# Kernel tuning notes

Measured on AMD Instinct MI355X. Metric: run time of the kernel, lower is better.

## Reference

```python
import jax, jax.numpy as jnp
import numpy as np

B, T, C, NH = 4, 2048, 1024, 16
D = C // NH  # 64


def setup_inputs() -> dict:
    key = jax.random.key(0)
    ks = jax.random.split(key, 6)
    x = jax.random.normal(ks[0], (B, T, C), dtype=jnp.float32)
    # realistic RoPE tables: interleaved cos/sin over T positions, D head dim
    inv_freq = 1.0 / (10000.0 ** (np.arange(0, D, 2, dtype=np.float32) / D))
    ang = np.arange(T, dtype=np.float32)[:, None] * inv_freq[None, :]  # (T, D/2)
    ang = np.repeat(ang, 2, axis=-1)  # (T, D) interleaved
    pe_cos = jnp.asarray(np.cos(ang))[None, None]  # (1,1,T,D)
    pe_sin = jnp.asarray(np.sin(ang))[None, None]
    pe_scale = jax.random.uniform(ks[1], (1, 1, T, D), dtype=jnp.float32, minval=0.5, maxval=1.5)
    mask = 0.1 * jax.random.normal(ks[2], (1, B, T, T), dtype=jnp.float32)
    w_qkv = jax.random.normal(ks[3], (3 * C, C), dtype=jnp.float32) * (C ** -0.5)
    b_qkv = jax.random.normal(ks[4], (3 * C,), dtype=jnp.float32) * 0.02
    return {"x": x, "pe_cos": pe_cos, "pe_sin": pe_sin, "pe_scale": pe_scale,
            "mask": mask, "w_qkv": w_qkv, "b_qkv": b_qkv}


def _rotate_interleaved(u):
    # even positions <- -odd, odd positions <- even (RoPE interleave)
    u2 = u.reshape(u.shape[:-1] + (-1, 2))
    rot = jnp.stack([-u2[..., 1], u2[..., 0]], axis=-1)
    return rot.reshape(u.shape)


def reference(x, pe_cos, pe_sin, pe_scale, mask, w_qkv, b_qkv):
    b, t, c = x.shape
    qkv = x @ w_qkv.T + b_qkv  # (b, t, 3c)
    q, k, v = jnp.split(qkv, 3, axis=-1)
    # (b, t, nh, d) -> (b, nh, t, d)
    to_heads = lambda u: u.reshape(b, t, NH, D).transpose(0, 2, 1, 3)
    q, k, v = to_heads(q), to_heads(k), to_heads(v)
    # pe tensors (1,1,t,d) broadcast over (b,nh,t,d)
    q = (q * pe_cos + _rotate_interleaved(q) * pe_sin) * pe_scale
    k = (k * pe_cos + _rotate_interleaved(k) * pe_sin) / pe_scale
    scale = 1.0 / ((2.0 * D) ** 0.5)  # original uses scale=1/sqrt(2d)
    scores = jnp.einsum('bhqd,bhkd->bhqk', q, k) * scale
    # torch layout was (nh, b, t, t) + mask (1, b, t, t): mask broadcasts over heads
    scores = scores + jnp.swapaxes(mask, 0, 1)  # mask -> (b, 1, t, t)
    attn = jax.nn.softmax(scores, axis=-1)
    out = jnp.einsum('bhqk,bhkd->bhqd', attn, v)  # (b, nh, t, d)
    return out.transpose(0, 2, 1, 3).reshape(b, t, c)
```

## Files before the change

kernel.cpp:

```cpp
#include <hip/hip_runtime.h>
#include <math.h>

#define NB 4
#define NT 2048
#define NC 1024
#define NHEADS 16
#define HDIM 64

typedef __attribute__((ext_vector_type(8))) _Float16 half8v;
typedef __attribute__((ext_vector_type(4))) float f32x4;

__device__ inline unsigned short f2h(float f) {
    _Float16 h = (_Float16)f;
    return __builtin_bit_cast(unsigned short, h);
}

#define AS1C(p) ((const __attribute__((address_space(1))) unsigned int*)(unsigned long long)(const void*)(p))
#define AS3P(p) ((__attribute__((address_space(3))) unsigned int*)(unsigned int)(unsigned long long)(void*)(p))
#define GLL16(gp, lp) __builtin_amdgcn_global_load_lds(AS1C(gp), AS3P(lp), 16, 0, 0)

__global__ __launch_bounds__(256) void conv_f16_kernel(
    const float* __restrict__ in, unsigned short* __restrict__ out, int n4)
{
    const int i = blockIdx.x * 256 + threadIdx.x;
    if (i >= n4) return;
    const float4 f = ((const float4*)in)[i];
    ushort4 h;
    h.x = f2h(f.x); h.y = f2h(f.y); h.z = f2h(f.z); h.w = f2h(f.w);
    ((ushort4*)out)[i] = h;
}

__global__ __launch_bounds__(256) void qkv_gemm_kernel(
    const unsigned short* __restrict__ xf, const unsigned short* __restrict__ wf,
    const float* __restrict__ bias, const float* __restrict__ pe_cos,
    const float* __restrict__ pe_sin, const float* __restrict__ pe_scale,
    unsigned short* __restrict__ qb, unsigned short* __restrict__ kb,
    unsigned short* __restrict__ vtb)
{
    __shared__ __align__(16) unsigned short Ah[128 * 32];
    __shared__ __align__(16) unsigned short Bh[128 * 32];

    const int tid = threadIdx.x;
    const int w = tid >> 6, lane = tid & 63;
    const int g = lane >> 4, fr = lane & 15;
    const int wr = w >> 1, wc = w & 1;

    const int bid = blockIdx.x;
    const int s = (bid & 7) * 192 + (bid >> 3);
    const int m0 = (s & 63) * 128, n0 = (s >> 6) * 128;

    const int c0 = tid, c1 = tid + 256;
    const int r0 = c0 >> 2, r1 = c1 >> 2;
    const int cb0 = ((c0 & 3) * 16) ^ (((r0 >> 1) & 3) << 4);
    const int cb1 = ((c1 & 3) * 16) ^ (((r1 >> 1) & 3) << 4);
    const unsigned short* px0 = xf + (size_t)(m0 + r0) * NC + (cb0 >> 1);
    const unsigned short* px1 = xf + (size_t)(m0 + r1) * NC + (cb1 >> 1);
    const unsigned short* pw0 = wf + (size_t)(n0 + r0) * NC + (cb0 >> 1);
    const unsigned short* pw1 = wf + (size_t)(n0 + r1) * NC + (cb1 >> 1);

    f32x4 acc[4][4];
#pragma unroll
    for (int m = 0; m < 4; ++m)
#pragma unroll
        for (int n = 0; n < 4; ++n) acc[m][n] = (f32x4){0.f, 0.f, 0.f, 0.f};

    for (int k0 = 0; k0 < NC; k0 += 32) {
        __syncthreads();
        GLL16(px0 + k0, (char*)Ah + c0 * 16);
        GLL16(px1 + k0, (char*)Ah + c1 * 16);
        GLL16(pw0 + k0, (char*)Bh + c0 * 16);
        GLL16(pw1 + k0, (char*)Bh + c1 * 16);
        __syncthreads();

        half8v a_f[4], b_f[4];
#pragma unroll
        for (int m = 0; m < 4; ++m) {
            const int r = wr * 64 + m * 16 + fr;
            const int off = r * 64 + ((g * 16) ^ (((r >> 1) & 3) << 4));
            a_f[m] = *(const half8v*)((const char*)Ah + off);
        }
#pragma unroll
        for (int n = 0; n < 4; ++n) {
            const int r = wc * 64 + n * 16 + fr;
            const int off = r * 64 + ((g * 16) ^ (((r >> 1) & 3) << 4));
            b_f[n] = *(const half8v*)((const char*)Bh + off);
        }
#pragma unroll
        for (int m = 0; m < 4; ++m)
#pragma unroll
            for (int n = 0; n < 4; ++n)
                acc[m][n] = __builtin_amdgcn_mfma_f32_16x16x32_f16(a_f[m], b_f[n], acc[m][n], 0, 0, 0);
    }

#pragma unroll
    for (int n = 0; n < 4; ++n) {
        const int col = n0 + wc * 64 + n * 16 + fr;
        const int part = col >> 10;
        const int hh = (col & 1023) >> 6;
        const int dd = col & 63;
        const float bv = bias[col];
#pragma unroll
        for (int m = 0; m < 4; ++m) {
            const int row0 = m0 + wr * 64 + m * 16 + 4 * g;
            const int bb = row0 >> 11;
            const int t0 = row0 & 2047;
            if (part < 2) {
                unsigned short* outp = (part == 0) ? qb : kb;
#pragma unroll
                for (int j = 0; j < 4; ++j) {
                    const int t = t0 + j;
                    float val = acc[m][n][j] + bv;
                    const float partner = __shfl_xor(val, 1, 64);
                    const int pidx = t * HDIM + dd;
                    const float cc = pe_cos[pidx], ss = pe_sin[pidx], sc = pe_scale[pidx];
                    const float r = (dd & 1) ? (val * cc + partner * ss)
                                             : (val * cc - partner * ss);
                    val = (part == 0) ? (r * sc) : (r / sc);
                    outp[(((size_t)bb * NHEADS + hh) * NT + t) * HDIM + dd] = f2h(val);
                }
            } else {
                ushort4 sv;
                sv.x = f2h(acc[m][n][0] + bv);
                sv.y = f2h(acc[m][n][1] + bv);
                sv.z = f2h(acc[m][n][2] + bv);
                sv.w = f2h(acc[m][n][3] + bv);
                *(ushort4*)&vtb[(((size_t)bb * NHEADS + hh) * HDIM + dd) * NT + t0] = sv;
            }
        }
    }
}

__global__ __launch_bounds__(256) void attn_mfma_kernel(
    const unsigned short* __restrict__ qb, const unsigned short* __restrict__ kb,
    const unsigned short* __restrict__ vtb, const float* __restrict__ mask,
    float* __restrict__ out)
{
    __shared__ __align__(16) unsigned short Qs[64 * 64];
    __shared__ __align__(16) unsigned short Ks[64 * 64];
    __shared__ __align__(16) unsigned short Vs[64 * 64];
    __shared__ __align__(16) unsigned short Ps[4][16 * 64];

    const int tid = threadIdx.x;
    const int w = tid >> 6, lane = tid & 63;
    const int g = lane >> 4, fr = lane & 15;

    const int bid = blockIdx.x;
    const int s = (bid & 7) * 256 + (bid >> 3);
    const int q0 = (s & 31) * 64;
    const int h = (s >> 5) & 15;
    const int b = s >> 9;

    const size_t bh = (size_t)b * NHEADS + h;
    const unsigned short* qp = qb + (bh * NT + q0) * HDIM;
    const unsigned short* kp = kb + bh * NT * HDIM;
    const unsigned short* vtp = vtb + bh * HDIM * NT;
    const float* mp = mask + ((size_t)b * NT + q0) * NT;

    {
        const int c0 = tid, c1 = tid + 256;
        const int r0 = c0 >> 3, cbq0 = ((c0 & 7) * 16) ^ ((r0 & 7) << 4);
        const int r1 = c1 >> 3, cbq1 = ((c1 & 7) * 16) ^ ((r1 & 7) << 4);
        GLL16(qp + r0 * HDIM + (cbq0 >> 1), (char*)Qs + c0 * 16);
        GLL16(qp + r1 * HDIM + (cbq1 >> 1), (char*)Qs + c1 * 16);
    }
    __syncthreads();
    half8v qf[2];
    {
        const int r = w * 16 + fr;
#pragma unroll
        for (int kk = 0; kk < 2; ++kk) {
            const int off = r * 128 + ((g * 16 + kk * 64) ^ ((r & 7) << 4));
            qf[kk] = *(const half8v*)((const char*)Qs + off);
        }
    }

    f32x4 acc[4];
    float li[4], mi[4];
#pragma unroll
    for (int j = 0; j < 4; ++j) {
        li[j] = 0.f; mi[j] = -3.0e38f;
        acc[j] = (f32x4){0.f, 0.f, 0.f, 0.f};
    }
    const float scl = 0.08838834764831845f;

    for (int kt = 0; kt < NT / 64; ++kt) {
        __syncthreads();
        {
            const unsigned short* ktp = kp + kt * 64 * HDIM;
#pragma unroll
            for (int half = 0; half < 2; ++half) {
                const int c = tid + half * 256;
                const int r = c >> 3;
                const int cb = ((c & 7) * 16) ^ ((r & 7) << 4);
                GLL16(ktp + r * HDIM + (cb >> 1), (char*)Ks + c * 16);
                GLL16(vtp + (size_t)r * NT + kt * 64 + (cb >> 1), (char*)Vs + c * 16);
            }
        }
        __syncthreads();

        f32x4 S[4];
#pragma unroll
        for (int nt = 0; nt < 4; ++nt) {
            S[nt] = (f32x4){0.f, 0.f, 0.f, 0.f};
            const int r = nt * 16 + fr;
#pragma unroll
            for (int kk = 0; kk < 2; ++kk) {
                const int off = r * 128 + ((g * 16 + kk * 64) ^ ((r & 7) << 4));
                const half8v kf = *(const half8v*)((const char*)Ks + off);
                S[nt] = __builtin_amdgcn_mfma_f32_16x16x32_f16(qf[kk], kf, S[nt], 0, 0, 0);
            }
        }

        float sv[4][4], rmj[4];
#pragma unroll
        for (int j = 0; j < 4; ++j) {
            const int qrow = w * 16 + 4 * g + j;
            const float* mrow = mp + (size_t)qrow * NT + kt * 64 + fr;
#pragma unroll
            for (int nt = 0; nt < 4; ++nt)
                sv[j][nt] = fmaf(S[nt][j], scl, mrow[nt * 16]);
            rmj[j] = fmaxf(fmaxf(sv[j][0], sv[j][1]), fmaxf(sv[j][2], sv[j][3]));
        }

        float worst = fmaxf(fmaxf(rmj[0] - mi[0], rmj[1] - mi[1]),
                            fmaxf(rmj[2] - mi[2], rmj[3] - mi[3]));
        if (!__all(worst <= 8.f)) {
#pragma unroll
            for (int j = 0; j < 4; ++j) {
                float rm = rmj[j];
                rm = fmaxf(rm, __shfl_xor(rm, 1, 64));
                rm = fmaxf(rm, __shfl_xor(rm, 2, 64));
                rm = fmaxf(rm, __shfl_xor(rm, 4, 64));
                rm = fmaxf(rm, __shfl_xor(rm, 8, 64));
                const float mnew = fmaxf(mi[j], rm);
                const float alpha = __expf(mi[j] - mnew);
                li[j] *= alpha;
                acc[0][j] *= alpha; acc[1][j] *= alpha;
                acc[2][j] *= alpha; acc[3][j] *= alpha;
                mi[j] = mnew;
            }
        }

#pragma unroll
        for (int j = 0; j < 4; ++j) {
            const int prow = 4 * g + j;
            float ps = 0.f;
#pragma unroll
            for (int nt = 0; nt < 4; ++nt) {
                const float p = __expf(sv[j][nt] - mi[j]);
                const int off = prow * 128 + ((nt * 32 + fr * 2) ^ ((prow & 7) << 4));
                *(unsigned short*)((char*)Ps[w] + off) = f2h(p);
                ps += p;
            }
            li[j] += ps;
        }

        half8v pf[2];
#pragma unroll
        for (int kk = 0; kk < 2; ++kk) {
            const int off = fr * 128 + ((g * 16 + kk * 64) ^ ((fr & 7) << 4));
            pf[kk] = *(const half8v*)((const char*)Ps[w] + off);
        }
#pragma unroll
        for (int dt = 0; dt < 4; ++dt) {
            const int d = dt * 16 + fr;
#pragma unroll
            for (int kk = 0; kk < 2; ++kk) {
                const int off = d * 128 + ((g * 16 + kk * 64) ^ ((d & 7) << 4));
                const half8v vf = *(const half8v*)((const char*)Vs + off);
                acc[dt] = __builtin_amdgcn_mfma_f32_16x16x32_f16(pf[kk], vf, acc[dt], 0, 0, 0);
            }
        }
    }

#pragma unroll
    for (int j = 0; j < 4; ++j) {
        float lt = li[j];
        lt += __shfl_xor(lt, 1, 64);
        lt += __shfl_xor(lt, 2, 64);
        lt += __shfl_xor(lt, 4, 64);
        lt += __shfl_xor(lt, 8, 64);
        const float inv = 1.f / lt;
        const int t = q0 + w * 16 + 4 * g + j;
        float* op = out + (((size_t)b * NT + t) * NHEADS + h) * HDIM;
#pragma unroll
        for (int dt = 0; dt < 4; ++dt) op[dt * 16 + fr] = acc[dt][j] * inv;
    }
}

extern "C" void kernel_launch(void* const* d_in, const int* in_sizes, int n_in,
                              void* d_out, int out_size, void* d_ws, size_t ws_size,
                              hipStream_t stream) {
    const float* x        = (const float*)d_in[0];
    const float* pe_cos   = (const float*)d_in[1];
    const float* pe_sin   = (const float*)d_in[2];
    const float* pe_scale = (const float*)d_in[3];
    const float* mask     = (const float*)d_in[4];
    const float* w_qkv    = (const float*)d_in[5];
    const float* b_qkv    = (const float*)d_in[6];
    float* out = (float*)d_out;

    unsigned short* ws = (unsigned short*)d_ws;
    const size_t PER = (size_t)NB * NHEADS * NT * HDIM;
    unsigned short* qbuf = ws;
    unsigned short* kbuf = ws + PER;
    unsigned short* vtbuf = ws + 2 * PER;
    unsigned short* xbuf = ws + 3 * PER;
    unsigned short* wbuf = ws + 4 * PER;

    conv_f16_kernel<<<8192, 256, 0, stream>>>(x, xbuf, (NB * NT * NC) / 4);
    conv_f16_kernel<<<3072, 256, 0, stream>>>(w_qkv, wbuf, (3 * NC * NC) / 4);
    qkv_gemm_kernel<<<1536, 256, 0, stream>>>(xbuf, wbuf, b_qkv,
                                              pe_cos, pe_sin, pe_scale,
                                              qbuf, kbuf, vtbuf);
    attn_mfma_kernel<<<2048, 256, 0, stream>>>(qbuf, kbuf, vtbuf, mask, out);
}
```

Before: 277.2 us.

## Enlarge attention Q tile to 256 rows per block and stream mask as fp16

Each wave now handles 64 query rows (four 16-row sub-tiles) instead of 16, so every K/V tile loaded into LDS is reused across four times as many queries. The grid drops from 2048 to 512 blocks, Q fragments load straight from global memory into registers, and launch bounds request two blocks per CU. The mask is converted to fp16 by an extra pass into the workspace region that held x, halving the attention kernel's mask reads. The trade-offs are a large register footprint from 16 accumulator tiles, fewer blocks for latency hiding, and an extra full read and write of the mask in the conversion kernel.

```diff
diff --git a/kernel.cpp b/kernel.cpp
--- a/kernel.cpp
+++ b/kernel.cpp
@@ -13,6 +13,9 @@
 __device__ inline unsigned short f2h(float f) {
     _Float16 h = (_Float16)f;
     return __builtin_bit_cast(unsigned short, h);
+}
+__device__ inline float h2f(unsigned short u) {
+    return (float)__builtin_bit_cast(_Float16, u);
 }
 
 #define AS1C(p) ((const __attribute__((address_space(1))) unsigned int*)(unsigned long long)(const void*)(p))
@@ -130,57 +133,47 @@
     }
 }
 
-__global__ __launch_bounds__(256) void attn_mfma_kernel(
+__global__ __launch_bounds__(256, 2) void attn_mfma_kernel(
     const unsigned short* __restrict__ qb, const unsigned short* __restrict__ kb,
-    const unsigned short* __restrict__ vtb, const float* __restrict__ mask,
+    const unsigned short* __restrict__ vtb, const unsigned short* __restrict__ m16,
     float* __restrict__ out)
 {
-    __shared__ __align__(16) unsigned short Qs[64 * 64];
     __shared__ __align__(16) unsigned short Ks[64 * 64];
     __shared__ __align__(16) unsigned short Vs[64 * 64];
-    __shared__ __align__(16) unsigned short Ps[4][16 * 64];
+    __shared__ __align__(16) unsigned short Ps[4][64 * 64];
 
     const int tid = threadIdx.x;
     const int w = tid >> 6, lane = tid & 63;
     const int g = lane >> 4, fr = lane & 15;
 
     const int bid = blockIdx.x;
-    const int s = (bid & 7) * 256 + (bid >> 3);
-    const int q0 = (s & 31) * 64;
-    const int h = (s >> 5) & 15;
-    const int b = s >> 9;
+    const int s = (bid & 7) * 64 + (bid >> 3);
+    const int q0 = (s & 7) * 256;
+    const int h = (s >> 3) & 15;
+    const int b = s >> 7;
 
     const size_t bh = (size_t)b * NHEADS + h;
-    const unsigned short* qp = qb + (bh * NT + q0) * HDIM;
+    const unsigned short* qp = qb + (bh * NT + q0 + w * 64) * HDIM;
     const unsigned short* kp = kb + bh * NT * HDIM;
     const unsigned short* vtp = vtb + bh * HDIM * NT;
-    const float* mp = mask + ((size_t)b * NT + q0) * NT;
-
-    {
-        const int c0 = tid, c1 = tid + 256;
-        const int r0 = c0 >> 3, cbq0 = ((c0 & 7) * 16) ^ ((r0 & 7) << 4);
-        const int r1 = c1 >> 3, cbq1 = ((c1 & 7) * 16) ^ ((r1 & 7) << 4);
-        GLL16(qp + r0 * HDIM + (cbq0 >> 1), (char*)Qs + c0 * 16);
-        GLL16(qp + r1 * HDIM + (cbq1 >> 1), (char*)Qs + c1 * 16);
-    }
-    __syncthreads();
-    half8v qf[2];
-    {
-        const int r = w * 16 + fr;
-#pragma unroll
-        for (int kk = 0; kk < 2; ++kk) {
-            const int off = r * 128 + ((g * 16 + kk * 64) ^ ((r & 7) << 4));
-            qf[kk] = *(const half8v*)((const char*)Qs + off);
-        }
-    }
-
-    f32x4 acc[4];
-    float li[4], mi[4];
-#pragma unroll
-    for (int j = 0; j < 4; ++j) {
-        li[j] = 0.f; mi[j] = -3.0e38f;
-        acc[j] = (f32x4){0.f, 0.f, 0.f, 0.f};
-    }
+    const unsigned short* mp = m16 + ((size_t)b * NT + q0 + w * 64) * NT;
+
+    half8v qf[4][2];
+#pragma unroll
+    for (int m = 0; m < 4; ++m)
+#pragma unroll
+        for (int kk = 0; kk < 2; ++kk)
+            qf[m][kk] = *(const half8v*)(qp + (m * 16 + fr) * HDIM + kk * 32 + g * 8);
+
+    f32x4 acc[4][4];
+    float li[4][4], mi[4][4];
+#pragma unroll
+    for (int m = 0; m < 4; ++m)
+#pragma unroll
+        for (int j = 0; j < 4; ++j) {
+            li[m][j] = 0.f; mi[m][j] = -3.0e38f;
+            acc[m][j] = (f32x4){0.f, 0.f, 0.f, 0.f};
+        }
     const float scl = 0.08838834764831845f;
 
     for (int kt = 0; kt < NT / 64; ++kt) {
@@ -198,94 +191,114 @@
         }
         __syncthreads();
 
-        f32x4 S[4];
+        half8v kf[4][2];
 #pragma unroll
         for (int nt = 0; nt < 4; ++nt) {
-            S[nt] = (f32x4){0.f, 0.f, 0.f, 0.f};
             const int r = nt * 16 + fr;
 #pragma unroll
             for (int kk = 0; kk < 2; ++kk) {
-                const int off = r * 128 + ((g * 16 + kk * 64) ^ ((r & 7) << 4));
-                const half8v kf = *(const half8v*)((const char*)Ks + off);
-                S[nt] = __builtin_amdgcn_mfma_f32_16x16x32_f16(qf[kk], kf, S[nt], 0, 0, 0);
-            }
-        }
-
-        float sv[4][4], rmj[4];
-#pragma unroll
-        for (int j = 0; j < 4; ++j) {
-            const int qrow = w * 16 + 4 * g + j;
-            const float* mrow = mp + (size_t)qrow * NT + kt * 64 + fr;
-#pragma unroll
-            for (int nt = 0; nt < 4; ++nt)
-                sv[j][nt] = fmaf(S[nt][j], scl, mrow[nt * 16]);
-            rmj[j] = fmaxf(fmaxf(sv[j][0], sv[j][1]), fmaxf(sv[j][2], sv[j][3]));
-        }
-
-        float worst = fmaxf(fmaxf(rmj[0] - mi[0], rmj[1] - mi[1]),
-                            fmaxf(rmj[2] - mi[2], rmj[3] - mi[3]));
-        if (!__all(worst <= 8.f)) {
+                const int off = r * 128 + ((kk * 64 + g * 16) ^ ((r & 7) << 4));
+                kf[nt][kk] = *(const half8v*)((const char*)Ks + off);
+            }
+        }
+
+#pragma unroll
+        for (int m = 0; m < 4; ++m) {
+            f32x4 Sm[4];
+#pragma unroll
+            for (int nt = 0; nt < 4; ++nt) {
+                Sm[nt] = (f32x4){0.f, 0.f, 0.f, 0.f};
+#pragma unroll
+                for (int kk = 0; kk < 2; ++kk)
+                    Sm[nt] = __builtin_amdgcn_mfma_f32_16x16x32_f16(qf[m][kk], kf[nt][kk], Sm[nt], 0, 0, 0);
+            }
+
+            float sv[4][4], rmj[4];
 #pragma unroll
             for (int j = 0; j < 4; ++j) {
-                float rm = rmj[j];
-                rm = fmaxf(rm, __shfl_xor(rm, 1, 64));
-                rm = fmaxf(rm, __shfl_xor(rm, 2, 64));
-                rm = fmaxf(rm, __shfl_xor(rm, 4, 64));
-                rm = fmaxf(rm, __shfl_xor(rm, 8, 64));
-                const float mnew = fmaxf(mi[j], rm);
-                const float alpha = __expf(mi[j] - mnew);
-                li[j] *= alpha;
-                acc[0][j] *= alpha; acc[1][j] *= alpha;
-                acc[2][j] *= alpha; acc[3][j] *= alpha;
-                mi[j] = mnew;
-            }
-        }
-
-#pragma unroll
-        for (int j = 0; j < 4; ++j) {
-            const int prow = 4 * g + j;
-            float ps = 0.f;
-#pragma unroll
-            for (int nt = 0; nt < 4; ++nt) {
-                const float p = __expf(sv[j][nt] - mi[j]);
-                const int off = prow * 128 + ((nt * 32 + fr * 2) ^ ((prow & 7) << 4));
-                *(unsigned short*)((char*)Ps[w] + off) = f2h(p);
-                ps += p;
-            }
-            li[j] += ps;
-        }
-
-        half8v pf[2];
-#pragma unroll
-        for (int kk = 0; kk < 2; ++kk) {
-            const int off = fr * 128 + ((g * 16 + kk * 64) ^ ((fr & 7) << 4));
-            pf[kk] = *(const half8v*)((const char*)Ps[w] + off);
-        }
+                const unsigned short* mrow =
+                    mp + (size_t)(m * 16 + 4 * g + j) * NT + kt * 64 + fr;
+#pragma unroll
+                for (int nt = 0; nt < 4; ++nt)
+                    sv[j][nt] = fmaf(Sm[nt][j], scl, h2f(mrow[nt * 16]));
+                rmj[j] = fmaxf(fmaxf(sv[j][0], sv[j][1]), fmaxf(sv[j][2], sv[j][3]));
+            }
+
+            const float worst = fmaxf(fmaxf(rmj[0] - mi[m][0], rmj[1] - mi[m][1]),
+                                      fmaxf(rmj[2] - mi[m][2], rmj[3] - mi[m][3]));
+            if (!__all(worst <= 8.f)) {
+#pragma unroll
+                for (int j = 0; j < 4; ++j) {
+                    float rm = rmj[j];
+                    rm = fmaxf(rm, __shfl_xor(rm, 1, 64));
+                    rm = fmaxf(rm, __shfl_xor(rm, 2, 64));
+                    rm = fmaxf(rm, __shfl_xor(rm, 4, 64));
+                    rm = fmaxf(rm, __shfl_xor(rm, 8, 64));
+                    const float mnew = fmaxf(mi[m][j], rm);
+                    const float alpha = __expf(mi[m][j] - mnew);
+                    li[m][j] *= alpha;
+#pragma unroll
+                    for (int dt = 0; dt < 4; ++dt) acc[m][dt][j] *= alpha;
+                    mi[m][j] = mnew;
+                }
+            }
+
+#pragma unroll
+            for (int j = 0; j < 4; ++j) {
+                const int prow = m * 16 + 4 * g + j;
+                float ps = 0.f;
+#pragma unroll
+                for (int nt = 0; nt < 4; ++nt) {
+                    const float p = __expf(sv[j][nt] - mi[m][j]);
+                    const int off = prow * 128 + ((nt * 32 + fr * 2) ^ ((prow & 7) << 4));
+                    *(unsigned short*)((char*)Ps[w] + off) = f2h(p);
+                    ps += p;
+                }
+                li[m][j] += ps;
+            }
+        }
+
+        half8v vf[4][2];
 #pragma unroll
         for (int dt = 0; dt < 4; ++dt) {
             const int d = dt * 16 + fr;
 #pragma unroll
             for (int kk = 0; kk < 2; ++kk) {
-                const int off = d * 128 + ((g * 16 + kk * 64) ^ ((d & 7) << 4));
-                const half8v vf = *(const half8v*)((const char*)Vs + off);
-                acc[dt] = __builtin_amdgcn_mfma_f32_16x16x32_f16(pf[kk], vf, acc[dt], 0, 0, 0);
-            }
+                const int off = d * 128 + ((kk * 64 + g * 16) ^ ((d & 7) << 4));
+                vf[dt][kk] = *(const half8v*)((const char*)Vs + off);
+            }
+        }
+#pragma unroll
+        for (int m = 0; m < 4; ++m) {
+            half8v pf[2];
+#pragma unroll
+            for (int kk = 0; kk < 2; ++kk) {
+                const int off = (m * 16 + fr) * 128 + ((kk * 64 + g * 16) ^ ((fr & 7) << 4));
+                pf[kk] = *(const half8v*)((const char*)Ps[w] + off);
+            }
+#pragma unroll
+            for (int dt = 0; dt < 4; ++dt)
+#pragma unroll
+                for (int kk = 0; kk < 2; ++kk)
+                    acc[m][dt] = __builtin_amdgcn_mfma_f32_16x16x32_f16(pf[kk], vf[dt][kk], acc[m][dt], 0, 0, 0);
         }
     }
 
 #pragma unroll
-    for (int j = 0; j < 4; ++j) {
-        float lt = li[j];
-        lt += __shfl_xor(lt, 1, 64);
-        lt += __shfl_xor(lt, 2, 64);
-        lt += __shfl_xor(lt, 4, 64);
-        lt += __shfl_xor(lt, 8, 64);
-        const float inv = 1.f / lt;
-        const int t = q0 + w * 16 + 4 * g + j;
-        float* op = out + (((size_t)b * NT + t) * NHEADS + h) * HDIM;
-#pragma unroll
-        for (int dt = 0; dt < 4; ++dt) op[dt * 16 + fr] = acc[dt][j] * inv;
-    }
+    for (int m = 0; m < 4; ++m)
+#pragma unroll
+        for (int j = 0; j < 4; ++j) {
+            float lt = li[m][j];
+            lt += __shfl_xor(lt, 1, 64);
+            lt += __shfl_xor(lt, 2, 64);
+            lt += __shfl_xor(lt, 4, 64);
+            lt += __shfl_xor(lt, 8, 64);
+            const float inv = 1.f / lt;
+            const int t = q0 + w * 64 + m * 16 + 4 * g + j;
+            float* op = out + (((size_t)b * NT + t) * NHEADS + h) * HDIM;
+#pragma unroll
+            for (int dt = 0; dt < 4; ++dt) op[dt * 16 + fr] = acc[m][dt][j] * inv;
+        }
 }
 
 extern "C" void kernel_launch(void* const* d_in, const int* in_sizes, int n_in,
@@ -306,12 +319,14 @@
     unsigned short* kbuf = ws + PER;
     unsigned short* vtbuf = ws + 2 * PER;
     unsigned short* xbuf = ws + 3 * PER;
-    unsigned short* wbuf = ws + 4 * PER;
+    unsigned short* wbuf = xbuf + (size_t)NB * NT * NC;
+    unsigned short* maskbuf = ws + 3 * PER;
 
     conv_f16_kernel<<<8192, 256, 0, stream>>>(x, xbuf, (NB * NT * NC) / 4);
     conv_f16_kernel<<<3072, 256, 0, stream>>>(w_qkv, wbuf, (3 * NC * NC) / 4);
     qkv_gemm_kernel<<<1536, 256, 0, stream>>>(xbuf, wbuf, b_qkv,
                                               pe_cos, pe_sin, pe_scale,
                                               qbuf, kbuf, vtbuf);
-    attn_mfma_kernel<<<2048, 256, 0, stream>>>(qbuf, kbuf, vtbuf, mask, out);
-}
+    conv_f16_kernel<<<16384, 256, 0, stream>>>(mask, maskbuf, (NB * NT * NT) / 4);
+    attn_mfma_kernel<<<512, 256, 0, stream>>>(qbuf, kbuf, vtbuf, maskbuf, out);
+}
```

Result: slower. 512.1 us (+84.8%).
